# Kernel tuning notes

Measured on AMD Instinct MI355X. Metric: run time of the kernel, lower is better.

## Reference

```python
import jax, jax.numpy as jnp
import numpy as np

P_DROP = 0.009

def setup_inputs() -> dict:
    key = jax.random.key(0)
    kq, kk, kv, ks = jax.random.split(key, 4)
    B, S, D = 4, 4096, 64
    q = jax.random.normal(kq, (B, S, D), dtype=jnp.float32)
    k = jax.random.normal(kk, (B, S, D), dtype=jnp.float32)
    v = jax.random.normal(kv, (B, S, D), dtype=jnp.float32)
    s = jax.random.uniform(ks, (1,), dtype=jnp.float32) + 0.5  # positive scalar divisor
    return {"q": q, "k": k, "v": v, "s": s}

def reference(q, k, v, s):
    # qk = q @ k^T / s  -> [B, S, S]
    qk = jnp.einsum('bqd,bkd->bqk', q, k) / s[0]
    p = jax.nn.softmax(qk, axis=-1)
    # dropout p=0.009 (training mode in the original F.dropout); fixed key for determinism
    keep = 1.0 - P_DROP
    mask = jax.random.bernoulli(jax.random.key(1), keep, p.shape)
    p = jnp.where(mask, p / keep, jnp.zeros((), p.dtype))
    # output = dropout(softmax) @ v -> [B, S, Dv]
    return jnp.einsum('bqk,bkd->bqd', p, v)
```

## Files before the change

### kernel.cpp

```cpp
#include <hip/hip_runtime.h>
#include <stdint.h>

#define S_LEN 4096
#define KEEP_P 0.991f

typedef __attribute__((ext_vector_type(8)))  short bf16x8;
typedef __attribute__((ext_vector_type(16))) float f32x16;
typedef __attribute__((ext_vector_type(4)))  int   i32x4;
typedef __attribute__((ext_vector_type(2)))  int   i32x2;

static constexpr uint32_t TOTAL_N    = 4u * 4096u * 4096u;
static constexpr uint32_t MASK_WORDS = TOTAL_N / 32u;
static constexpr uint32_t KEEP_TH = 4256312832u;

#define TFR_AB(sh) { v0 += v1; uint32_t d_;                                  \
  asm("v_alignbit_b32 %0, %1, %1, " #sh : "=v"(d_) : "v"(v1));               \
  v1 = d_ ^ v0; }

__device__ __forceinline__ void threefry(uint32_t x0, uint32_t x1,
                                         uint32_t& o0, uint32_t& o1) {
  const uint32_t k0 = 0u, k1 = 1u, k2 = 0x1BD11BDBu;
  uint32_t v0 = x0 + k0, v1 = x1 + k1;
  TFR_AB(19) TFR_AB(17) TFR_AB(6) TFR_AB(26)
  v0 += k1; v1 += k2 + 1u;
  TFR_AB(15) TFR_AB(3) TFR_AB(16) TFR_AB(8)
  v0 += k2; v1 += k0 + 2u;
  TFR_AB(19) TFR_AB(17) TFR_AB(6) TFR_AB(26)
  v0 += k0; v1 += k1 + 3u;
  TFR_AB(15) TFR_AB(3) TFR_AB(16) TFR_AB(8)
  v0 += k1; v1 += k2 + 4u;
  TFR_AB(19) TFR_AB(17) TFR_AB(6) TFR_AB(26)
  v0 += k2; v1 += k0 + 5u;
  o0 = v0; o1 = v1;
}

__device__ __forceinline__ bool keep_partitionable(uint32_t i) {
  uint32_t o0, o1;
  threefry(0u, i, o0, o1);
  return (o0 ^ o1) < KEEP_TH;
}

__global__ __launch_bounds__(256) void maskgen_kernel(uint32_t* __restrict__ mask) {
  uint32_t gid  = blockIdx.x * 256u + threadIdx.x;
  uint32_t base = gid * 32u;
  uint32_t wlo = 0u, whi = 0u;
#pragma unroll
  for (uint32_t j = 0; j < 16u; ++j) {
    uint32_t a0, a1, b0, b1;
    threefry(0u, base + j,        a0, a1);
    threefry(0u, base + j + 16u,  b0, b1);
    wlo |= (uint32_t)((a0 ^ a1) < KEEP_TH) << j;
    whi |= (uint32_t)((b0 ^ b1) < KEEP_TH) << j;
  }
  mask[gid] = wlo | (whi << 16);
}

__device__ __forceinline__ uint32_t f2u(float f){ union{float f;uint32_t u;}x; x.f=f; return x.u; }
__device__ __forceinline__ float u2f(uint32_t u){ union{uint32_t u;float f;}x; x.u=u; return x.f; }

template<bool USE_WS>
__global__ __launch_bounds__(512, 2)
void attn_mfma(const float* __restrict__ Qg, const float* __restrict__ Kg,
               const float* __restrict__ Vg, const float* __restrict__ Sdiv,
               const uint32_t* __restrict__ Mask, float* __restrict__ Out)
{
  __shared__ __align__(16) unsigned char smem[49152];
  __shared__ float sm_ml[2][3][2][32];
  char* khiB = (char*)smem;
  char* kloB = (char*)smem + 16384;
  char* vtsB = (char*)smem + 32768;
  float* smf = (float*)smem;

  const int t    = threadIdx.x;
  const int lane = t & 63;
  const int w    = t >> 6;
  const int wq   = w >> 2;
  const int h    = w & 3;
  const int l31  = lane & 31;
  const int hi5  = lane >> 5;

  const int blk = blockIdx.x;
  const int xcd = blk & 7;
  const int b   = xcd >> 1;
  const int qblock = ((xcd & 1) << 5) | (blk >> 3);
  const int qt  = qblock * 64;

  const float inv_s = 1.0f / Sdiv[0];
  const float* Qp = Qg + (size_t)b * S_LEN * 64;
  const float* Kp = Kg + (size_t)b * S_LEN * 64;
  const float* Vp = Vg + (size_t)b * S_LEN * 64;

#pragma unroll
  for (int rr = 0; rr < 2; ++rr) {
    int row = rr * 32 + (t >> 4);
    int c   = (t & 15) * 4;
    float4 q4 = *(const float4*)(Qp + (size_t)(qt + row) * 64 + c);
    uint32_t u0=f2u(q4.x),u1=f2u(q4.y),u2=f2u(q4.z),u3=f2u(q4.w);
    uint32_t h01=(u1&0xFFFF0000u)|(u0>>16), h23=(u3&0xFFFF0000u)|(u2>>16);
    uint32_t l0=f2u(q4.x-u2f(u0&0xFFFF0000u)), l1=f2u(q4.y-u2f(u1&0xFFFF0000u));
    uint32_t l2=f2u(q4.z-u2f(u2&0xFFFF0000u)), l3=f2u(q4.w-u2f(u3&0xFFFF0000u));
    uint32_t lo01=(l1&0xFFFF0000u)|(l0>>16), lo23=(l3&0xFFFF0000u)|(l2>>16);
    uint32_t off = ((uint32_t)(row*128 + c*2)) ^ ((uint32_t)((row&7)<<4));
    *(i32x2*)(khiB + off) = i32x2{(int)h01,(int)h23};
    *(i32x2*)(kloB + off) = i32x2{(int)lo01,(int)lo23};
  }
  __syncthreads();
  bf16x8 qhi[4], qlo[4];
  {
    int qrow = wq * 32 + l31;
#pragma unroll
    for (int kc = 0; kc < 4; ++kc) {
      uint32_t off = ((uint32_t)(qrow*128 + kc*32 + hi5*16)) ^ ((uint32_t)((qrow&7)<<4));
      qhi[kc] = *(const bf16x8*)(khiB + off);
      qlo[kc] = *(const bf16x8*)(kloB + off);
    }
  }
  __syncthreads();

  f32x16 o0, o1;
#pragma unroll
  for (int i = 0; i < 16; ++i) { o0[i] = 0.f; o1[i] = 0.f; }
  float m = -INFINITY, lsum = 0.f;

  const int rowk = h * 32 + l31;
  const uint32_t qglob = (uint32_t)(qt + wq * 32 + l31);
  const uint32_t mrowbase = ((uint32_t)b * 4096u + qglob) * 128u;

  union PU { i32x4 i; bf16x8 bv; };

  for (int kt0 = 0; kt0 < S_LEN; kt0 += 128) {
#pragma unroll
    for (int rr = 0; rr < 4; ++rr) {
      int row = rr * 32 + (t >> 4);
      int c   = (t & 15) * 4;
      float4 k4 = *(const float4*)(Kp + (size_t)(kt0 + row) * 64 + c);
      uint32_t u0=f2u(k4.x),u1=f2u(k4.y),u2=f2u(k4.z),u3=f2u(k4.w);
      uint32_t h01=(u1&0xFFFF0000u)|(u0>>16), h23=(u3&0xFFFF0000u)|(u2>>16);
      uint32_t l0=f2u(k4.x-u2f(u0&0xFFFF0000u)), l1=f2u(k4.y-u2f(u1&0xFFFF0000u));
      uint32_t l2=f2u(k4.z-u2f(u2&0xFFFF0000u)), l3=f2u(k4.w-u2f(u3&0xFFFF0000u));
      uint32_t lo01=(l1&0xFFFF0000u)|(l0>>16), lo23=(l3&0xFFFF0000u)|(l2>>16);
      uint32_t off = ((uint32_t)(row*128 + c*2)) ^ ((uint32_t)((row&7)<<4));
      *(i32x2*)(khiB + off) = i32x2{(int)h01,(int)h23};
      *(i32x2*)(kloB + off) = i32x2{(int)lo01,(int)lo23};

      float4 v4 = *(const float4*)(Vp + (size_t)(kt0 + row) * 64 + c);
      uint32_t vp01, vp23;
      asm("v_cvt_pk_bf16_f32 %0, %1, %2" : "=v"(vp01) : "v"(v4.x), "v"(v4.y));
      asm("v_cvt_pk_bf16_f32 %0, %1, %2" : "=v"(vp23) : "v"(v4.z), "v"(v4.w));
      *(i32x2*)(vtsB + (uint32_t)(row*128 + c*2)) = i32x2{(int)vp01,(int)vp23};
    }
    __syncthreads();

    uint32_t mw;
    if constexpr (USE_WS) {
      mw = Mask[mrowbase + (uint32_t)((kt0 + h * 32) >> 5)];
    } else {
      uint32_t fb = (((uint32_t)b*4096u + qglob)*4096u) + (uint32_t)(kt0 + h*32);
      mw = 0u;
      for (uint32_t j = 0; j < 32u; ++j) mw |= (uint32_t)keep_partitionable(fb + j) << j;
    }

    f32x16 acc;
#pragma unroll
    for (int i = 0; i < 16; ++i) acc[i] = 0.f;
    bf16x8 kfrag[4];
    const uint32_t kswz = (uint32_t)((rowk&7)<<4);
#pragma unroll
    for (int kc = 0; kc < 4; ++kc) {
      uint32_t off = ((uint32_t)(rowk*128 + kc*32 + hi5*16)) ^ kswz;
      kfrag[kc] = *(const bf16x8*)(khiB + off);
    }
#pragma unroll
    for (int kc = 0; kc < 4; ++kc)
      acc = __builtin_amdgcn_mfma_f32_32x32x16_bf16(kfrag[kc], qhi[kc], acc, 0, 0, 0);
#pragma unroll
    for (int kc = 0; kc < 4; ++kc)
      acc = __builtin_amdgcn_mfma_f32_32x32x16_bf16(kfrag[kc], qlo[kc], acc, 0, 0, 0);
#pragma unroll
    for (int kc = 0; kc < 4; ++kc) {
      uint32_t off = ((uint32_t)(rowk*128 + kc*32 + hi5*16)) ^ kswz;
      kfrag[kc] = *(const bf16x8*)(kloB + off);
    }
#pragma unroll
    for (int kc = 0; kc < 4; ++kc)
      acc = __builtin_amdgcn_mfma_f32_32x32x16_bf16(kfrag[kc], qhi[kc], acc, 0, 0, 0);

    float z[16];
#pragma unroll
    for (int i = 0; i < 16; ++i) z[i] = acc[i] * inv_s;
    float tmax = z[0];
#pragma unroll
    for (int i = 1; i < 16; ++i) tmax = fmaxf(tmax, z[i]);
    tmax = fmaxf(tmax, __shfl_xor(tmax, 32));
    float mn = fmaxf(m, tmax);
    if (!__all(mn == m)) {
      float cr = __expf(m - mn);
      m = mn;
      lsum *= cr;
#pragma unroll
      for (int r = 0; r < 16; ++r) {
        int qr = (r & 3) + 8 * (r >> 2) + 4 * hi5;
        float cq = __shfl(cr, qr);
        o0[r] *= cq; o1[r] *= cq;
      }
    }
    float em[16];
#pragma unroll
    for (int r = 0; r < 16; ++r) {
      float e = __expf(z[r] - m);
      lsum += e;
      int bit = (r & 3) + 8 * (r >> 2) + 4 * hi5;
      em[r] = ((mw >> bit) & 1u) ? e : 0.f;
    }

    uint32_t cw[8];
#pragma unroll
    for (int i = 0; i < 8; ++i)
      asm("v_cvt_pk_bf16_f32 %0, %1, %2" : "=v"(cw[i]) : "v"(em[2*i]), "v"(em[2*i+1]));
    uint32_t sx[8];
#pragma unroll
    for (int i = 0; i < 8; ++i) sx[i] = (uint32_t)__shfl_xor((int)cw[i], 32);
    PU pf0, pf1;
    pf0.i = i32x4{ (int)(hi5 ? sx[2] : cw[0]),
                   (int)(hi5 ? sx[3] : cw[1]),
                   (int)(hi5 ? cw[2] : sx[0]),
                   (int)(hi5 ? cw[3] : sx[1]) };
    pf1.i = i32x4{ (int)(hi5 ? sx[6] : cw[4]),
                   (int)(hi5 ? sx[7] : cw[5]),
                   (int)(hi5 ? cw[6] : sx[4]),
                   (int)(hi5 ? cw[7] : sx[5]) };

    PU vf00, vf01, vf10, vf11;
#pragma unroll
    for (int ks = 0; ks < 2; ++ks)
#pragma unroll
      for (int vb = 0; vb < 2; ++vb) {
        int wds[4];
#pragma unroll
        for (int jj = 0; jj < 4; ++jj) {
          int k0 = 32*h + 16*ks + 8*hi5 + 2*jj;
          uint32_t lo = *(const uint16_t*)(vtsB + k0*128     + (vb*32 + l31)*2);
          uint32_t hi = *(const uint16_t*)(vtsB + (k0+1)*128 + (vb*32 + l31)*2);
          wds[jj] = (int)(lo | (hi << 16));
        }
        PU tmp; tmp.i = i32x4{wds[0], wds[1], wds[2], wds[3]};
        if (ks == 0 && vb == 0) vf00 = tmp;
        else if (ks == 0 && vb == 1) vf01 = tmp;
        else if (ks == 1 && vb == 0) vf10 = tmp;
        else vf11 = tmp;
      }

    o0 = __builtin_amdgcn_mfma_f32_32x32x16_bf16(pf0.bv, vf00.bv, o0, 0, 0, 0);
    o0 = __builtin_amdgcn_mfma_f32_32x32x16_bf16(pf1.bv, vf10.bv, o0, 0, 0, 0);
    o1 = __builtin_amdgcn_mfma_f32_32x32x16_bf16(pf0.bv, vf01.bv, o1, 0, 0, 0);
    o1 = __builtin_amdgcn_mfma_f32_32x32x16_bf16(pf1.bv, vf11.bv, o1, 0, 0, 0);
    __syncthreads();
  }

  lsum += __shfl_xor(lsum, 32);
  if (h > 0) {
    if (lane < 32) { sm_ml[wq][h-1][0][l31] = m; sm_ml[wq][h-1][1][l31] = lsum; }
    float* dst = smf + (size_t)(wq * 3 + (h - 1)) * 2048;
#pragma unroll
    for (int r = 0; r < 16; ++r) {
      int qr = (r & 3) + 8 * (r >> 2) + 4 * hi5;
      dst[qr * 64 + l31]      = o0[r];
      dst[qr * 64 + 32 + l31] = o1[r];
    }
  }
  __syncthreads();
  if (h == 0) {
#pragma unroll
    for (int hp = 1; hp < 4; ++hp) {
      float mp = sm_ml[wq][hp-1][0][l31];
      float lp = sm_ml[wq][hp-1][1][l31];
      float mm = fmaxf(m, mp);
      float ca = __expf(m - mm);
      float cb = __expf(mp - mm);
      lsum = lsum * ca + lp * cb;
      m = mm;
      const float* srcp = smf + (size_t)(wq * 3 + (hp - 1)) * 2048;
#pragma unroll
      for (int r = 0; r < 16; ++r) {
        int qr = (r & 3) + 8 * (r >> 2) + 4 * hi5;
        float caq = __shfl(ca, qr);
        float cbq = __shfl(cb, qr);
        o0[r] = o0[r] * caq + srcp[qr * 64 + l31] * cbq;
        o1[r] = o1[r] * caq + srcp[qr * 64 + 32 + l31] * cbq;
      }
    }
    float rinv = 1.0f / (lsum * KEEP_P);
    float* op = Out + ((size_t)b * S_LEN + (size_t)(qt + wq * 32)) * 64;
#pragma unroll
    for (int r = 0; r < 16; ++r) {
      int qr = (r & 3) + 8 * (r >> 2) + 4 * hi5;
      float rq = __shfl(rinv, qr);
      op[(size_t)qr * 64 + l31]      = o0[r] * rq;
      op[(size_t)qr * 64 + 32 + l31] = o1[r] * rq;
    }
  }
}

extern "C" void kernel_launch(void* const* d_in, const int* in_sizes, int n_in,
                              void* d_out, int out_size, void* d_ws, size_t ws_size,
                              hipStream_t stream) {
  (void)in_sizes; (void)n_in; (void)out_size;
  const float* q = (const float*)d_in[0];
  const float* k = (const float*)d_in[1];
  const float* v = (const float*)d_in[2];
  const float* s = (const float*)d_in[3];
  float* out = (float*)d_out;

  const bool use_ws = ws_size >= (size_t)MASK_WORDS * sizeof(uint32_t);
  if (use_ws) {
    uint32_t* mask = (uint32_t*)d_ws;
    maskgen_kernel<<<MASK_WORDS / 256u, 256, 0, stream>>>(mask);
    attn_mfma<true><<<dim3(256), dim3(512), 0, stream>>>(q, k, v, s, mask, out);
  } else {
    attn_mfma<false><<<dim3(256), dim3(512), 0, stream>>>(q, k, v, s, nullptr, out);
  }
}
```

Baseline: 180.6 us.

## Fuse dropout mask generation into attention via producer waves with double-buffered LDS

Removes the separate mask-generation kernel and its global mask buffer. The attention kernel gets 256 extra producer threads that compute the Threefry keep-bits for the next 128-key tile into a double-buffered LDS array. They stay in step with the compute waves through matching __syncthreads calls, so the hashing overlaps the MFMA work and the mask is never written to or read from global memory. In exchange the block grows to 768 threads with launch bounds (768,3), which caps registers per thread and risks spills in the MFMA path. The producer's barrier count must also match the consumer loop exactly.

```diff
diff --git a/kernel.cpp b/kernel.cpp
--- a/kernel.cpp
+++ b/kernel.cpp
@@ -9,8 +9,6 @@
 typedef __attribute__((ext_vector_type(4)))  int   i32x4;
 typedef __attribute__((ext_vector_type(2)))  int   i32x2;
 
-static constexpr uint32_t TOTAL_N    = 4u * 4096u * 4096u;
-static constexpr uint32_t MASK_WORDS = TOTAL_N / 32u;
 static constexpr uint32_t KEEP_TH = 4256312832u;
 
 #define TFR_AB(sh) { v0 += v1; uint32_t d_;                                  \
@@ -34,56 +32,81 @@
   o0 = v0; o1 = v1;
 }
 
-__device__ __forceinline__ bool keep_partitionable(uint32_t i) {
-  uint32_t o0, o1;
-  threefry(0u, i, o0, o1);
-  return (o0 ^ o1) < KEEP_TH;
-}
-
-__global__ __launch_bounds__(256) void maskgen_kernel(uint32_t* __restrict__ mask) {
-  uint32_t gid  = blockIdx.x * 256u + threadIdx.x;
-  uint32_t base = gid * 32u;
-  uint32_t wlo = 0u, whi = 0u;
-#pragma unroll
-  for (uint32_t j = 0; j < 16u; ++j) {
-    uint32_t a0, a1, b0, b1;
-    threefry(0u, base + j,        a0, a1);
-    threefry(0u, base + j + 16u,  b0, b1);
-    wlo |= (uint32_t)((a0 ^ a1) < KEEP_TH) << j;
-    whi |= (uint32_t)((b0 ^ b1) < KEEP_TH) << j;
-  }
-  mask[gid] = wlo | (whi << 16);
-}
-
 __device__ __forceinline__ uint32_t f2u(float f){ union{float f;uint32_t u;}x; x.f=f; return x.u; }
 __device__ __forceinline__ float u2f(uint32_t u){ union{uint32_t u;float f;}x; x.u=u; return x.f; }
 
-template<bool USE_WS>
-__global__ __launch_bounds__(512, 2)
-void attn_mfma(const float* __restrict__ Qg, const float* __restrict__ Kg,
-               const float* __restrict__ Vg, const float* __restrict__ Sdiv,
-               const uint32_t* __restrict__ Mask, float* __restrict__ Out)
+__global__ __launch_bounds__(768, 3)
+void fused_attn(const float* __restrict__ Qg, const float* __restrict__ Kg,
+                const float* __restrict__ Vg, const float* __restrict__ Sdiv,
+                float* __restrict__ Out)
 {
   __shared__ __align__(16) unsigned char smem[49152];
   __shared__ float sm_ml[2][3][2][32];
+  __shared__ uint32_t mbuf[2][64][4];
+
+  const int t = threadIdx.x;
+
+  const int blk = blockIdx.x;
+  const int xcd = blk & 7;
+  const int b   = xcd >> 1;
+  const int qblock = ((xcd & 1) << 5) | (blk >> 3);
+  const int qt  = qblock * 64;
+
+  if (t >= 512) {
+    const int p    = t - 512;
+    const int row  = p >> 2;
+    const int word = p & 3;
+    const uint32_t fb0 = (((uint32_t)b * 4096u + (uint32_t)(qt + row)) << 12)
+                       + ((uint32_t)word << 5);
+
+    {
+      uint32_t wlo = 0u, whi = 0u;
+#pragma unroll
+      for (uint32_t j = 0; j < 16u; ++j) {
+        uint32_t a0, a1, b0, b1;
+        threefry(0u, fb0 + j,        a0, a1);
+        threefry(0u, fb0 + j + 16u,  b0, b1);
+        wlo |= (uint32_t)((a0 ^ a1) < KEEP_TH) << j;
+        whi |= (uint32_t)((b0 ^ b1) < KEEP_TH) << j;
+      }
+      mbuf[0][row][word] = wlo | (whi << 16);
+    }
+    __syncthreads();
+    __syncthreads();
+
+#pragma unroll 1
+    for (int tt = 0; tt < 32; ++tt) {
+      if (tt < 31) {
+        const uint32_t fb = fb0 + (uint32_t)((tt + 1) << 7);
+        uint32_t wlo = 0u, whi = 0u;
+#pragma unroll
+        for (uint32_t j = 0; j < 16u; ++j) {
+          uint32_t a0, a1, b0, b1;
+          threefry(0u, fb + j,        a0, a1);
+          threefry(0u, fb + j + 16u,  b0, b1);
+          wlo |= (uint32_t)((a0 ^ a1) < KEEP_TH) << j;
+          whi |= (uint32_t)((b0 ^ b1) < KEEP_TH) << j;
+        }
+        mbuf[(tt + 1) & 1][row][word] = wlo | (whi << 16);
+      }
+      __syncthreads();
+      __syncthreads();
+    }
+    __syncthreads();
+    return;
+  }
+
   char* khiB = (char*)smem;
   char* kloB = (char*)smem + 16384;
   char* vtsB = (char*)smem + 32768;
   float* smf = (float*)smem;
 
-  const int t    = threadIdx.x;
   const int lane = t & 63;
   const int w    = t >> 6;
   const int wq   = w >> 2;
   const int h    = w & 3;
   const int l31  = lane & 31;
   const int hi5  = lane >> 5;
-
-  const int blk = blockIdx.x;
-  const int xcd = blk & 7;
-  const int b   = xcd >> 1;
-  const int qblock = ((xcd & 1) << 5) | (blk >> 3);
-  const int qt  = qblock * 64;
 
   const float inv_s = 1.0f / Sdiv[0];
   const float* Qp = Qg + (size_t)b * S_LEN * 64;
@@ -123,8 +146,6 @@
   float m = -INFINITY, lsum = 0.f;
 
   const int rowk = h * 32 + l31;
-  const uint32_t qglob = (uint32_t)(qt + wq * 32 + l31);
-  const uint32_t mrowbase = ((uint32_t)b * 4096u + qglob) * 128u;
 
   union PU { i32x4 i; bf16x8 bv; };
 
@@ -151,14 +172,7 @@
     }
     __syncthreads();
 
-    uint32_t mw;
-    if constexpr (USE_WS) {
-      mw = Mask[mrowbase + (uint32_t)((kt0 + h * 32) >> 5)];
-    } else {
-      uint32_t fb = (((uint32_t)b*4096u + qglob)*4096u) + (uint32_t)(kt0 + h*32);
-      mw = 0u;
-      for (uint32_t j = 0; j < 32u; ++j) mw |= (uint32_t)keep_partitionable(fb + j) << j;
-    }
+    const uint32_t mw = mbuf[(kt0 >> 7) & 1][wq * 32 + l31][h];
 
     f32x16 acc;
 #pragma unroll
@@ -304,19 +318,12 @@
 extern "C" void kernel_launch(void* const* d_in, const int* in_sizes, int n_in,
                               void* d_out, int out_size, void* d_ws, size_t ws_size,
                               hipStream_t stream) {
-  (void)in_sizes; (void)n_in; (void)out_size;
+  (void)in_sizes; (void)n_in; (void)out_size; (void)d_ws; (void)ws_size;
   const float* q = (const float*)d_in[0];
   const float* k = (const float*)d_in[1];
   const float* v = (const float*)d_in[2];
   const float* s = (const float*)d_in[3];
   float* out = (float*)d_out;
 
-  const bool use_ws = ws_size >= (size_t)MASK_WORDS * sizeof(uint32_t);
-  if (use_ws) {
-    uint32_t* mask = (uint32_t*)d_ws;
-    maskgen_kernel<<<MASK_WORDS / 256u, 256, 0, stream>>>(mask);
-    attn_mfma<true><<<dim3(256), dim3(512), 0, stream>>>(q, k, v, s, mask, out);
-  } else {
-    attn_mfma<false><<<dim3(256), dim3(512), 0, stream>>>(q, k, v, s, nullptr, out);
-  }
+  fused_attn<<<dim3(256), dim3(768), 0, stream>>>(q, k, v, s, out);
 }
```

New measurement: 205.6 us. 13.9% more time.
